# Optimization experiments

Measured on AMD Instinct MI355X. Metric: run time of the kernel, lower is better.

Reference implementation:

```python
import jax, jax.numpy as jnp
import numpy as np

B, CV, CP, X, Y, Z = 4, 16, 16, 256, 256, 32
NV, NORIG, NSLOT, D = 100000, 131072, 50, 256
CC = CV + CP  # combined_feature_dim = 32


def _l2norm(x, axis):
    n = jnp.linalg.norm(x, axis=axis, keepdims=True)
    return x / jnp.maximum(n, 1e-12)


def _group_norm(x, gamma, beta, groups=4, eps=1e-5):
    # x: [B, C, L]; normalize over (C//groups, L) per group, like nn.GroupNorm
    b, c, l = x.shape
    xg = x.reshape(b, groups, c // groups, l)
    mu = xg.mean(axis=(2, 3), keepdims=True)
    var = xg.var(axis=(2, 3), keepdims=True)
    xg = (xg - mu) / jnp.sqrt(var + eps)
    return xg.reshape(b, c, l) * gamma[None, :, None] + beta[None, :, None]


def setup_inputs() -> dict:
    key = jax.random.key(0)
    ks = jax.random.split(key, 10)
    voxel_feats_dense = jax.random.normal(ks[0], (B, CV, X, Y, Z), dtype=jnp.float32)
    raw_point_feats = jax.random.normal(ks[1], (B, NV, CP), dtype=jnp.float32)
    slot = jax.random.normal(ks[2], (B, NSLOT, D), dtype=jnp.float32)
    # voxel_coords columns: [:,0] indexes Z, [:,1] indexes Y, [:,2] indexes X
    c0 = jax.random.randint(ks[3], (B, NV), 0, Z)
    c1 = jax.random.randint(ks[4], (B, NV), 0, Y)
    c2 = jax.random.randint(ks[5], (B, NV), 0, X)
    voxel_coords = jnp.stack([c0, c1, c2], axis=-1).astype(jnp.int32)
    # unique scatter targets per batch (voxelizer keeps a subset of raw points)
    point_idxes = jnp.stack([
        jax.random.permutation(jax.random.fold_in(ks[6], i), NORIG)[:NV]
        for i in range(B)
    ]).astype(jnp.int32)
    W1 = jax.random.normal(ks[7], (D, D), dtype=jnp.float32) * 0.05
    b1 = jnp.zeros((D,), jnp.float32)
    gn_gamma = jnp.ones((D,), jnp.float32)
    gn_beta = jnp.zeros((D,), jnp.float32)
    W2 = jax.random.normal(ks[8], (CC, D), dtype=jnp.float32) * 0.05
    b2 = jnp.zeros((CC,), jnp.float32)
    return dict(voxel_feats_dense=voxel_feats_dense, raw_point_feats=raw_point_feats,
                slot=slot, W1=W1, b1=b1, gn_gamma=gn_gamma, gn_beta=gn_beta,
                W2=W2, b2=b2, voxel_coords=voxel_coords, point_idxes=point_idxes,
                n_original=NORIG)


def reference(voxel_feats_dense, raw_point_feats, slot, W1, b1, gn_gamma, gn_beta,
              W2, b2, voxel_coords, point_idxes, n_original):
    b, cv, xd, yd, zd = voxel_feats_dense.shape
    vc = voxel_coords
    # voxel-to-point gather: dense[i, :, vc[:,2], vc[:,1], vc[:,0]].T
    lin = vc[..., 2] * (yd * zd) + vc[..., 1] * zd + vc[..., 0]  # [B, NV]
    flat = voxel_feats_dense.reshape(b, cv, -1)
    interp = jnp.take_along_axis(flat, lin[:, None, :], axis=2)  # [B, CV, NV]
    padded_feats = jnp.concatenate([jnp.transpose(interp, (0, 2, 1)),
                                    raw_point_feats], axis=-1)   # [B, NV, CC]
    # object_mlp on slot.transpose(1,2): conv1d(k=1) -> GroupNorm(4) -> ReLU -> conv1d(k=1)
    st = jnp.transpose(slot, (0, 2, 1))                           # [B, D, NSLOT]
    h = jnp.einsum('oc,bcn->bon', W1, st) + b1[None, :, None]
    h = jax.nn.relu(_group_norm(h, gn_gamma, gn_beta))
    slot_proj = jnp.einsum('oc,bcn->bon', W2, h) + b2[None, :, None]  # [B, CC, NSLOT]
    # cosine similarity mask with temperature 0.05
    mask = jnp.einsum('bnc,bck->bnk', _l2norm(padded_feats, 2),
                      _l2norm(slot_proj, 1)) / 0.05                # [B, NV, NSLOT]
    k = mask.shape[2]
    # scatter back to original point indices (zeros elsewhere)
    scatter = jax.vmap(lambda m, idx: jnp.zeros((n_original, k), m.dtype).at[idx].set(m))(
        mask, point_idxes)                                         # [B, NORIG, NSLOT]
    final = jnp.transpose(scatter.reshape(b * n_original, k), (1, 0))  # [NSLOT, B*NORIG]
    return jax.nn.softmax(final, axis=0)
```

## Files before the change

### kernel.cpp

```cpp
#include <hip/hip_runtime.h>

#define BB     4
#define CVC    16
#define CPC    16
#define CCC    32
#define XD     256
#define YD     256
#define ZD     32
#define NVX    100000
#define NORIG  131072
#define NSLOT  50
#define DD     256
#define XYZ    (XD*YD*ZD)
#define BN     ((size_t)BB*NORIG)

__global__ __launch_bounds__(256) void fill_kernel(int2* __restrict__ il,
                                                   float* __restrict__ stats){
  int i = blockIdx.x*256 + threadIdx.x;
  if (i < (int)BN) il[i] = make_int2(-1, 0);
  if (i < 32) stats[i] = 0.f;
}

__global__ __launch_bounds__(256) void scatter_kernel(const int* __restrict__ pidx,
                                                      const int* __restrict__ coords,
                                                      int2* __restrict__ il){
  int t = blockIdx.x*256 + threadIdx.x;
  if (t < BB*NVX){
    int b = t / NVX;
    int n = t - b*NVX;
    const int* vc = coords + 3*(size_t)t;
    int lin = vc[2]*(YD*ZD) + vc[1]*ZD + vc[0];
    il[(size_t)b*NORIG + pidx[t]] = make_int2(n, lin);
  }
}

__global__ __launch_bounds__(256) void mlp1_kernel(
    const float* __restrict__ slot, const float* __restrict__ W1,
    const float* __restrict__ b1, float* __restrict__ ws_h,
    float* __restrict__ stats){
  int s = blockIdx.x, b = blockIdx.y, d = threadIdx.x;
  __shared__ float sv[DD];
  sv[d] = slot[((size_t)b*NSLOT + s)*DD + d];
  __syncthreads();
  const float4* w1q = (const float4*)(W1 + (size_t)d*DD);
  float acc = b1[d];
  #pragma unroll
  for (int q = 0; q < 64; q++){
    float4 w = w1q[q];
    const float* sp = &sv[q*4];
    acc = fmaf(w.x, sp[0], acc);
    acc = fmaf(w.y, sp[1], acc);
    acc = fmaf(w.z, sp[2], acc);
    acc = fmaf(w.w, sp[3], acc);
  }
  ws_h[((size_t)b*NSLOT + s)*DD + d] = acc;
  float s1 = acc, s2 = acc*acc;
  #pragma unroll
  for (int off = 32; off > 0; off >>= 1){
    s1 += __shfl_down(s1, off, 64);
    s2 += __shfl_down(s2, off, 64);
  }
  if ((d & 63) == 0){
    int g = d >> 6;
    atomicAdd(&stats[(b*4+g)*2+0], s1);
    atomicAdd(&stats[(b*4+g)*2+1], s2);
  }
}

__global__ __launch_bounds__(256) void mlp2_kernel(
    const float* __restrict__ ws_h, const float* __restrict__ stats,
    const float* __restrict__ gamma, const float* __restrict__ beta,
    const float* __restrict__ W2, const float* __restrict__ b2,
    float* __restrict__ slotn){
  int s = blockIdx.x, b = blockIdx.y, d = threadIdx.x;
  float h = ws_h[((size_t)b*NSLOT + s)*DD + d];
  int g = d >> 6;
  float s1 = stats[(b*4+g)*2+0];
  float s2 = stats[(b*4+g)*2+1];
  const float invN = 1.f/3200.f;
  float mean = s1*invN;
  float var  = s2*invN - mean*mean;
  float hn = (h - mean) * rsqrtf(var + 1e-5f) * gamma[d] + beta[d];
  hn = fmaxf(hn, 0.f);
  __shared__ float hsh[DD];
  __shared__ float red[256];
  __shared__ float spo[CCC];
  hsh[d] = hn;
  __syncthreads();
  int o = d & 31, ch = d >> 5;
  const float4* w2q = (const float4*)(W2 + (size_t)o*DD + ch*32);
  float p = 0.f;
  #pragma unroll
  for (int q = 0; q < 8; q++){
    float4 w = w2q[q];
    const float* hp = &hsh[ch*32 + q*4];
    p = fmaf(w.x, hp[0], p);
    p = fmaf(w.y, hp[1], p);
    p = fmaf(w.z, hp[2], p);
    p = fmaf(w.w, hp[3], p);
  }
  red[d] = p;
  __syncthreads();
  if (ch == 0){
    float sp = b2[o];
    #pragma unroll
    for (int c = 0; c < 8; c++) sp += red[c*32 + o];
    spo[o] = sp;
  }
  __syncthreads();
  if (d < CCC){
    float ss = 0.f;
    #pragma unroll
    for (int o2 = 0; o2 < CCC; o2++) ss += spo[o2]*spo[o2];
    float sc = 20.f / fmaxf(sqrtf(ss), 1e-12f);
    slotn[((size_t)b*NSLOT + s)*CCC + d] = spo[d]*sc;
  }
}

__global__ __launch_bounds__(256, 6) void main_kernel(
    const float* __restrict__ vox, const float* __restrict__ raw,
    const int2* __restrict__ il, const float* __restrict__ slotn,
    float* __restrict__ out){
  int b = blockIdx.y;
  int col = blockIdx.x*256 + threadIdx.x;
  int2 t = il[(size_t)b*NORIG + col];
  float* op = out + (size_t)b*NORIG + col;
  int n = t.x;
  if (n >= 0){
    const float* vb = vox + (size_t)b*CVC*XYZ + (size_t)t.y;
    float f[CCC];
    #pragma unroll
    for (int c = 0; c < CVC; c++) f[c] = vb[(size_t)c*XYZ];
    const float4* rp = (const float4*)(raw + (size_t)CPC*((size_t)b*NVX + n));
    float4 q0 = rp[0], q1 = rp[1], q2 = rp[2], q3 = rp[3];
    f[16] = q0.x; f[17] = q0.y; f[18] = q0.z; f[19] = q0.w;
    f[20] = q1.x; f[21] = q1.y; f[22] = q1.z; f[23] = q1.w;
    f[24] = q2.x; f[25] = q2.y; f[26] = q2.z; f[27] = q2.w;
    f[28] = q3.x; f[29] = q3.y; f[30] = q3.z; f[31] = q3.w;
    float ss = 0.f;
    #pragma unroll
    for (int i = 0; i < CCC; i++) ss = fmaf(f[i], f[i], ss);
    float invn = 1.f / fmaxf(sqrtf(ss), 1e-12f);
    #pragma unroll
    for (int i = 0; i < CCC; i++) f[i] *= invn;
    const float* sb = slotn + (size_t)b*NSLOT*CCC;
    float sum = 0.f;
    #pragma unroll
    for (int k = 0; k < NSLOT; k++){
      const float4* sp = (const float4*)(sb + k*CCC);
      float acc = 0.f;
      #pragma unroll
      for (int q = 0; q < 8; q++){
        float4 v = sp[q];
        acc = fmaf(f[q*4+0], v.x, acc);
        acc = fmaf(f[q*4+1], v.y, acc);
        acc = fmaf(f[q*4+2], v.z, acc);
        acc = fmaf(f[q*4+3], v.w, acc);
      }
      sum += __expf(acc);
    }
    float rs = 1.f / sum;
    #pragma unroll
    for (int k = 0; k < NSLOT; k++){
      const float4* sp = (const float4*)(sb + k*CCC);
      float acc = 0.f;
      #pragma unroll
      for (int q = 0; q < 8; q++){
        float4 v = sp[q];
        acc = fmaf(f[q*4+0], v.x, acc);
        acc = fmaf(f[q*4+1], v.y, acc);
        acc = fmaf(f[q*4+2], v.z, acc);
        acc = fmaf(f[q*4+3], v.w, acc);
      }
      op[(size_t)k*BN] = __expf(acc) * rs;
    }
  } else {
    #pragma unroll
    for (int k = 0; k < NSLOT; k++) op[(size_t)k*BN] = 0.02f;
  }
}

extern "C" void kernel_launch(void* const* d_in, const int* in_sizes, int n_in,
                              void* d_out, int out_size, void* d_ws, size_t ws_size,
                              hipStream_t stream) {
  (void)in_sizes; (void)n_in; (void)out_size; (void)ws_size;
  const float* vox    = (const float*)d_in[0];
  const float* raw    = (const float*)d_in[1];
  const float* slot   = (const float*)d_in[2];
  const float* W1     = (const float*)d_in[3];
  const float* b1     = (const float*)d_in[4];
  const float* gamma  = (const float*)d_in[5];
  const float* beta   = (const float*)d_in[6];
  const float* W2     = (const float*)d_in[7];
  const float* b2     = (const float*)d_in[8];
  const int*   coords = (const int*)d_in[9];
  const int*   pidx   = (const int*)d_in[10];
  float*       out    = (float*)d_out;

  int2*  il    = (int2*)d_ws;
  float* stats = (float*)((char*)d_ws + BN*sizeof(int2));
  float* slotn = stats + 32;
  float* ws_h  = slotn + (size_t)BB*NSLOT*CCC;

  fill_kernel   <<<dim3((unsigned)((BN + 255)/256)), 256, 0, stream>>>(il, stats);
  scatter_kernel<<<dim3((BB*NVX + 255)/256),          256, 0, stream>>>(pidx, coords, il);
  mlp1_kernel   <<<dim3(NSLOT, BB),                   256, 0, stream>>>(slot, W1, b1, ws_h, stats);
  mlp2_kernel   <<<dim3(NSLOT, BB),                   256, 0, stream>>>(ws_h, stats, gamma, beta, W2, b2, slotn);
  main_kernel   <<<dim3(NORIG/256, BB),               256, 0, stream>>>(vox, raw, il, slotn, out);
}
```

Baseline: 959.3 us.

## Split slot dimension across four waves per column with shared-memory softmax reduction

The main kernel now gives each column to four wavefronts, and each wave computes a quarter of the 50 slot dot products. The exp values are kept in registers so the second pass that recomputed the dot products is gone. Partial softmax sums are combined through shared memory with one barrier. Invalid columns now go through the same path with a zeroed feature vector, which yields the uniform 0.02 output instead of a branch. In exchange, each of the four waves repeats the 32-channel gather (four times the vox/raw load traffic, likely served by cache), the code adds a block barrier, and the occupancy hint from launch bounds is dropped.

```diff
diff --git a/kernel.cpp b/kernel.cpp
--- a/kernel.cpp
+++ b/kernel.cpp
@@ -117,37 +117,45 @@
   }
 }
 
-__global__ __launch_bounds__(256, 6) void main_kernel(
+__global__ __launch_bounds__(256) void main_kernel(
     const float* __restrict__ vox, const float* __restrict__ raw,
     const int2* __restrict__ il, const float* __restrict__ slotn,
     float* __restrict__ out){
+  __shared__ float psum[4][64];
   int b = blockIdx.y;
-  int col = blockIdx.x*256 + threadIdx.x;
+  int w = threadIdx.x >> 6;
+  int l = threadIdx.x & 63;
+  int col = blockIdx.x*64 + l;
   int2 t = il[(size_t)b*NORIG + col];
-  float* op = out + (size_t)b*NORIG + col;
   int n = t.x;
-  if (n >= 0){
-    const float* vb = vox + (size_t)b*CVC*XYZ + (size_t)t.y;
-    float f[CCC];
-    #pragma unroll
-    for (int c = 0; c < CVC; c++) f[c] = vb[(size_t)c*XYZ];
-    const float4* rp = (const float4*)(raw + (size_t)CPC*((size_t)b*NVX + n));
-    float4 q0 = rp[0], q1 = rp[1], q2 = rp[2], q3 = rp[3];
-    f[16] = q0.x; f[17] = q0.y; f[18] = q0.z; f[19] = q0.w;
-    f[20] = q1.x; f[21] = q1.y; f[22] = q1.z; f[23] = q1.w;
-    f[24] = q2.x; f[25] = q2.y; f[26] = q2.z; f[27] = q2.w;
-    f[28] = q3.x; f[29] = q3.y; f[30] = q3.z; f[31] = q3.w;
-    float ss = 0.f;
-    #pragma unroll
-    for (int i = 0; i < CCC; i++) ss = fmaf(f[i], f[i], ss);
-    float invn = 1.f / fmaxf(sqrtf(ss), 1e-12f);
-    #pragma unroll
-    for (int i = 0; i < CCC; i++) f[i] *= invn;
-    const float* sb = slotn + (size_t)b*NSLOT*CCC;
-    float sum = 0.f;
-    #pragma unroll
-    for (int k = 0; k < NSLOT; k++){
-      const float4* sp = (const float4*)(sb + k*CCC);
+  float valid = (n >= 0) ? 1.f : 0.f;
+  int nn = (n < 0) ? 0 : n;
+  const float* vb = vox + (size_t)b*CVC*XYZ + (size_t)t.y;
+  float f[CCC];
+  #pragma unroll
+  for (int c = 0; c < CVC; c++) f[c] = vb[(size_t)c*XYZ];
+  const float4* rp = (const float4*)(raw + (size_t)CPC*((size_t)b*NVX + nn));
+  float4 q0 = rp[0], q1 = rp[1], q2 = rp[2], q3 = rp[3];
+  f[16] = q0.x; f[17] = q0.y; f[18] = q0.z; f[19] = q0.w;
+  f[20] = q1.x; f[21] = q1.y; f[22] = q1.z; f[23] = q1.w;
+  f[24] = q2.x; f[25] = q2.y; f[26] = q2.z; f[27] = q2.w;
+  f[28] = q3.x; f[29] = q3.y; f[30] = q3.z; f[31] = q3.w;
+  float ss = 0.f;
+  #pragma unroll
+  for (int i = 0; i < CCC; i++) ss = fmaf(f[i], f[i], ss);
+  float invn = valid / fmaxf(sqrtf(ss), 1e-12f);
+  #pragma unroll
+  for (int i = 0; i < CCC; i++) f[i] *= invn;
+  int k0 = (w*NSLOT) >> 2;
+  int k1 = ((w+1)*NSLOT) >> 2;
+  const float* sb = slotn + (size_t)b*NSLOT*CCC;
+  float e[13];
+  float ps = 0.f;
+  #pragma unroll
+  for (int kk = 0; kk < 13; kk++){
+    int k = k0 + kk;
+    if (k < k1){
+      const float4* sp = (const float4*)(sb + (size_t)k*CCC);
       float acc = 0.f;
       #pragma unroll
       for (int q = 0; q < 8; q++){
@@ -157,26 +165,19 @@
         acc = fmaf(f[q*4+2], v.z, acc);
         acc = fmaf(f[q*4+3], v.w, acc);
       }
-      sum += __expf(acc);
+      e[kk] = __expf(acc);
+      ps += e[kk];
     }
-    float rs = 1.f / sum;
-    #pragma unroll
-    for (int k = 0; k < NSLOT; k++){
-      const float4* sp = (const float4*)(sb + k*CCC);
-      float acc = 0.f;
-      #pragma unroll
-      for (int q = 0; q < 8; q++){
-        float4 v = sp[q];
-        acc = fmaf(f[q*4+0], v.x, acc);
-        acc = fmaf(f[q*4+1], v.y, acc);
-        acc = fmaf(f[q*4+2], v.z, acc);
-        acc = fmaf(f[q*4+3], v.w, acc);
-      }
-      op[(size_t)k*BN] = __expf(acc) * rs;
-    }
-  } else {
-    #pragma unroll
-    for (int k = 0; k < NSLOT; k++) op[(size_t)k*BN] = 0.02f;
+  }
+  psum[w][l] = ps;
+  __syncthreads();
+  float tot = psum[0][l] + psum[1][l] + psum[2][l] + psum[3][l];
+  float rs = 1.f / tot;
+  float* op = out + (size_t)b*NORIG + col;
+  #pragma unroll
+  for (int kk = 0; kk < 13; kk++){
+    int k = k0 + kk;
+    if (k < k1) op[(size_t)k*BN] = e[kk] * rs;
   }
 }
 
@@ -206,5 +207,5 @@
   scatter_kernel<<<dim3((BB*NVX + 255)/256),          256, 0, stream>>>(pidx, coords, il);
   mlp1_kernel   <<<dim3(NSLOT, BB),                   256, 0, stream>>>(slot, W1, b1, ws_h, stats);
   mlp2_kernel   <<<dim3(NSLOT, BB),                   256, 0, stream>>>(ws_h, stats, gamma, beta, W2, b2, slotn);
-  main_kernel   <<<dim3(NORIG/256, BB),               256, 0, stream>>>(vox, raw, il, slotn, out);
-}
+  main_kernel   <<<dim3(NORIG/64, BB),                256, 0, stream>>>(vox, raw, il, slotn, out);
+}
```

After: 894.9 us. 6.7% less time.
